# Optimization experiments

Measured on AMD Instinct MI355X. Metric: run time of the kernel, lower is better.

## Reference

```python
import jax, jax.numpy as jnp
import numpy as np

N = 4096          # batch size
D = 1024          # embedding dim
NUM_INSTANCES = 8 # samples per class (balanced batch, required by the original resize logic)
ALPHA = 20.0
MARGIN = 0.5


def setup_inputs() -> dict:
    key = jax.random.key(0)
    inputs = jax.random.normal(key, (N, D), dtype=jnp.float32)
    # balanced targets: each class appears exactly NUM_INSTANCES times
    targets = (jnp.arange(N, dtype=jnp.int32) // NUM_INSTANCES).astype(jnp.int32)
    return {"inputs": inputs, "targets": targets}


def reference(inputs, targets):
    n = inputs.shape[0]
    k_pos = NUM_INSTANCES - 1          # positives per row (excl. self)
    k_neg = n - NUM_INSTANCES          # negatives per row

    # L2 normalize rows, cosine similarity matrix [n, n]
    x = inputs / jnp.linalg.norm(inputs, axis=1, keepdims=True)
    sim = x @ x.T

    same = targets[:, None] == targets[None, :]
    eye = jnp.eye(n, dtype=bool)
    pos_mask = same & ~eye             # positives, diag removed
    neg_mask = ~same                   # negatives

    INF = jnp.float32(1e9)
    # per-row sorted positive / negative sims (ascending); fixed-size slices
    pos_sorted = jnp.sort(jnp.where(pos_mask, sim, INF), axis=1)[:, :k_pos]   # [n, k_pos]
    neg_sorted = jnp.sort(jnp.where(neg_mask, sim, INF), axis=1)[:, :k_neg]   # [n, k_neg]

    # base = max(max(sim) - 0.1, margin + 0.2)
    base = jnp.maximum(jnp.max(sim) - 0.1, MARGIN + 0.2)

    # dynamic selection expressed as masks over fixed-size sorted arrays
    neg_keep = neg_sorted > (pos_sorted[:, :1] - 0.05)   # negatives above min positive - 0.05
    pos_keep = pos_sorted < base                          # positives below base

    pos_elem = jnp.log1p(jnp.exp(-2.0 * (pos_sorted - MARGIN)))   # [n, k_pos]
    neg_elem = jnp.log1p(jnp.exp(ALPHA * (neg_sorted - MARGIN)))  # [n, k_neg]

    pos_cnt = pos_keep.sum(axis=1)
    neg_cnt = neg_keep.sum(axis=1)

    pos_mean = (pos_elem * pos_keep).sum(axis=1) / jnp.maximum(pos_cnt, 1).astype(sim.dtype)
    neg_mean = (neg_elem * neg_keep).sum(axis=1) / jnp.maximum(neg_cnt, 1).astype(sim.dtype)

    # fallbacks: empty pos set -> smallest positive; empty neg set -> largest negative
    pos_loss = jnp.where(pos_cnt > 0, pos_mean, pos_elem[:, 0])
    neg_loss = jnp.where(neg_cnt > 0, neg_mean, neg_elem[:, -1])

    return jnp.mean(pos_loss + neg_loss)   # sum over rows / n
```

## Files before the change

kernel.cpp:

```cpp
#include <hip/hip_runtime.h>
#include <hip/hip_bf16.h>
#include <hip/hip_fp8.h>
#include <math.h>

#define N 4096
#define D 1024
#define NINST 8
#define NGROUP (N / NINST)
#define ALPHA 20.0f
#define MARGIN 0.5f
#define NB 64
#define NTILE (NB * (NB + 1) / 2)

typedef __attribute__((ext_vector_type(4))) float f32x4;

__device__ __forceinline__ unsigned fkey(float f) {
    int b = __float_as_int(f);
    return (b >= 0) ? ((unsigned)b | 0x80000000u) : ~(unsigned)b;
}
__device__ __forceinline__ float fdec(unsigned u) {
    int b = (u & 0x80000000u) ? (int)(u ^ 0x80000000u) : ~(int)u;
    return __int_as_float(b);
}

__device__ __forceinline__ float softplus(float x) {
    float z = __expf(-fabsf(x));
    return fmaxf(x, 0.0f) + __logf(1.0f + z);
}

__device__ __forceinline__ void gld16(const void* g, void* l) {
    __builtin_amdgcn_global_load_lds(
        (const __attribute__((address_space(1))) void*)g,
        (__attribute__((address_space(3))) void*)l, 16, 0, 0);
}

__global__ __launch_bounds__(256) void k_normpos(const float* __restrict__ in,
                                                 unsigned long* __restrict__ xn8,
                                                 float* __restrict__ pos_sims,
                                                 float* __restrict__ min_pos,
                                                 unsigned* __restrict__ gmax,
                                                 float* __restrict__ accum,
                                                 unsigned* __restrict__ cnt) {
    __shared__ float4 srows4[8 * 257];
    __shared__ float spart[8][4];
    __shared__ float sinv[8];
    __shared__ float sg[8][8];

    int g = blockIdx.x;
    int t = threadIdx.x;
    int lane = t & 63, wid = t >> 6;

    if (g == 0) {
        if (t == 0) { *gmax = 0u; *cnt = 0u; }
        if (t < 32) accum[t] = 0.f;
    }

    const float4* in4 = (const float4*)in;
    #pragma unroll
    for (int i = 0; i < 8; ++i) {
        float4 v = in4[(size_t)g * 2048 + i * 256 + t];
        srows4[i * 257 + t] = v;
        float ss = v.x * v.x + v.y * v.y + v.z * v.z + v.w * v.w;
        #pragma unroll
        for (int off = 1; off < 64; off <<= 1) ss += __shfl_xor(ss, off);
        if (lane == 0) spart[i][wid] = ss;
    }
    __syncthreads();
    if (t < 8) sinv[t] = rsqrtf(spart[t][0] + spart[t][1] + spart[t][2] + spart[t][3]);
    __syncthreads();

    {
        int i_row = t & 7;
        int oct  = (t >> 3) & 3;
        int k0b  = t >> 5;
        size_t base = (size_t)(g >> 3) * 8192 + (size_t)((g >> 1) & 3) * 64
                    + (size_t)(oct * 16 + (g & 1) * 8 + i_row);
        float inv = sinv[i_row];
        #pragma unroll
        for (int j = 0; j < 4; ++j) {
            int k0 = k0b + j * 8;
            float4 v0 = srows4[i_row * 257 + k0 * 8 + oct * 2];
            float4 v1 = srows4[i_row * 257 + k0 * 8 + oct * 2 + 1];
            union { unsigned char c[8]; unsigned long u64; } o;
            o.c[0] = __hip_fp8_e4m3(v0.x * inv).__x;
            o.c[1] = __hip_fp8_e4m3(v0.y * inv).__x;
            o.c[2] = __hip_fp8_e4m3(v0.z * inv).__x;
            o.c[3] = __hip_fp8_e4m3(v0.w * inv).__x;
            o.c[4] = __hip_fp8_e4m3(v1.x * inv).__x;
            o.c[5] = __hip_fp8_e4m3(v1.y * inv).__x;
            o.c[6] = __hip_fp8_e4m3(v1.z * inv).__x;
            o.c[7] = __hip_fp8_e4m3(v1.w * inv).__x;
            xn8[base + (size_t)k0 * 256] = o.u64;
        }
    }

    int pair = t >> 2, a = pair >> 3, b = pair & 7, slice = t & 3;
    const float4* pa = srows4 + a * 257 + slice * 64;
    const float4* pb = srows4 + b * 257 + slice * 64;
    int j0 = (pair + slice * 2) & 63;
    float s = 0.f;
    #pragma unroll 8
    for (int i = 0; i < 64; ++i) {
        int j = (i + j0) & 63;
        float4 x = pa[j], y = pb[j];
        s += x.x * y.x + x.y * y.y + x.z * y.z + x.w * y.w;
    }
    s += __shfl_xor(s, 1);
    s += __shfl_xor(s, 2);
    if (slice == 0) sg[a][b] = s * sinv[a] * sinv[b];
    __syncthreads();
    if (t < 8) {
        float mn = 1e30f;
        int idx = 0;
        #pragma unroll
        for (int b2 = 0; b2 < 8; ++b2) {
            if (b2 == t) continue;
            float v = sg[t][b2];
            mn = fminf(mn, v);
            pos_sims[(size_t)(g * 8 + t) * 8 + idx] = v;
            ++idx;
        }
        min_pos[g * 8 + t] = mn;
    }
}

__global__ __launch_bounds__(256, 2) void k_neg(const unsigned long* __restrict__ xn8,
                                                const float* __restrict__ min_pos,
                                                float* __restrict__ sum_part,
                                                int* __restrict__ cnt_part,
                                                float* __restrict__ max_part,
                                                unsigned* __restrict__ gmax) {
    __shared__ char sbuf[4][3][4096];

    int t = threadIdx.x;
    int w = t >> 6;
    int l = t & 63;
    int u = blockIdx.x * 4 + w;

    int rt = 0, rem = u;
    while (rem >= NB - rt) { rem -= NB - rt; ++rt; }
    int ct = rt + rem;
    bool diag = (rt == ct);

    int R0 = rt * 64, C0 = ct * 64;
    int lrow = l & 15;
    int kgrp = l >> 4;

    float mA = min_pos[R0 + l];
    float mB = min_pos[C0 + l];
    asm volatile("s_waitcnt vmcnt(0)" ::: "memory");

    const char* xb = (const char*)xn8;
    const char* gA = xb + (size_t)rt * 65536 + (size_t)l * 16;
    const char* gB = xb + (size_t)ct * 65536 + (size_t)l * 16;
    char* ring = &sbuf[w][0][0];

    #define STAGE(s_)                                                   \
        do {                                                            \
            char* d_ = ring + ((s_) % 3) * 4096;                        \
            gld16(gA + (size_t)(s_) * 2048,        d_);                 \
            gld16(gA + (size_t)(s_) * 2048 + 1024, d_ + 1024);          \
            gld16(gB + (size_t)(s_) * 2048,        d_ + 2048);          \
            gld16(gB + (size_t)(s_) * 2048 + 1024, d_ + 3072);          \
        } while (0)

    STAGE(0); STAGE(1); STAGE(2);

    f32x4 zero = {0.f, 0.f, 0.f, 0.f};
    f32x4 acc[4][4];
    #pragma unroll
    for (int m = 0; m < 4; ++m)
        #pragma unroll
        for (int n = 0; n < 4; ++n) acc[m][n] = zero;

    for (int it = 0; it < 32; ++it) {
        if (it <= 29)      asm volatile("s_waitcnt vmcnt(8)" ::: "memory");
        else if (it == 30) asm volatile("s_waitcnt vmcnt(4)" ::: "memory");
        else               asm volatile("s_waitcnt vmcnt(0)" ::: "memory");

        const char* buf = ring + (it % 3) * 4096;
        long a[4], b[4];
        #pragma unroll
        for (int m = 0; m < 4; ++m) {
            a[m] = *(const long*)(buf + m * 512 + l * 8);
            b[m] = *(const long*)(buf + 2048 + m * 512 + l * 8);
        }

        #pragma unroll
        for (int m = 0; m < 4; ++m)
            #pragma unroll
            for (int n = 0; n < 4; ++n)
                acc[m][n] = __builtin_amdgcn_mfma_f32_16x16x32_fp8_fp8(
                    a[m], b[n], acc[m][n], 0, 0, 0);

        asm volatile("s_waitcnt lgkmcnt(0)" ::: "memory");
        if (it <= 28) STAGE(it + 3);
    }
    #undef STAGE

    float allmax = -1e30f;

    float thB[4];
    #pragma unroll
    for (int n = 0; n < 4; ++n) thB[n] = __shfl(mB, n * 16 + lrow) - 0.05f;

    float colS[4] = {0.f, 0.f, 0.f, 0.f};
    float colM[4] = {-1e30f, -1e30f, -1e30f, -1e30f};
    int   colC[4] = {0, 0, 0, 0};

    #pragma unroll
    for (int m = 0; m < 4; ++m) {
        #pragma unroll
        for (int reg = 0; reg < 4; ++reg) {
            int lr = m * 16 + kgrp * 4 + reg;
            int grow = R0 + lr;
            float th = __shfl(mA, lr) - 0.05f;
            int gi = grow >> 3;
            float rs = 0.f, rm = -1e30f;
            int rc = 0;
            #pragma unroll
            for (int n = 0; n < 4; ++n) {
                int gcol = C0 + n * 16 + lrow;
                float s = acc[m][n][reg];
                allmax = fmaxf(allmax, s);
                if ((gcol >> 3) != gi) {
                    float e = softplus(ALPHA * (s - MARGIN));
                    rm = fmaxf(rm, s);
                    if (s > th) { rs += e; rc += 1; }
                    if (!diag) {
                        colM[n] = fmaxf(colM[n], s);
                        if (s > thB[n]) { colS[n] += e; colC[n] += 1; }
                    }
                }
            }
            #pragma unroll
            for (int off = 1; off < 16; off <<= 1) {
                rs += __shfl_xor(rs, off);
                rc += __shfl_xor(rc, off);
                rm = fmaxf(rm, __shfl_xor(rm, off));
            }
            if (lrow == 0) {
                sum_part[(size_t)grow * 64 + ct] = rs;
                cnt_part[(size_t)grow * 64 + ct] = rc;
                max_part[(size_t)grow * 64 + ct] = rm;
            }
        }
    }

    if (!diag) {
        #pragma unroll
        for (int n = 0; n < 4; ++n) {
            float cs = colS[n], cm = colM[n];
            int cc = colC[n];
            cs += __shfl_xor(cs, 16); cs += __shfl_xor(cs, 32);
            cc += __shfl_xor(cc, 16); cc += __shfl_xor(cc, 32);
            cm = fmaxf(cm, __shfl_xor(cm, 16));
            cm = fmaxf(cm, __shfl_xor(cm, 32));
            if (kgrp == 0) {
                int gcol = C0 + n * 16 + lrow;
                sum_part[(size_t)gcol * 64 + rt] = cs;
                cnt_part[(size_t)gcol * 64 + rt] = cc;
                max_part[(size_t)gcol * 64 + rt] = cm;
            }
        }
    }

    #pragma unroll
    for (int off = 1; off < 64; off <<= 1) allmax = fmaxf(allmax, __shfl_xor(allmax, off));
    if (l == 0) atomicMax(gmax, fkey(allmax));
}

__global__ __launch_bounds__(256) void k_rowfinal(const float* __restrict__ sum_part,
                                                  const int* __restrict__ cnt_part,
                                                  const float* __restrict__ max_part,
                                                  const float* __restrict__ pos_sims,
                                                  const float* __restrict__ min_pos,
                                                  const unsigned* __restrict__ gmax,
                                                  float* __restrict__ accum,
                                                  unsigned* __restrict__ cnt,
                                                  float* __restrict__ out) {
    __shared__ float sloss[4];
    int row = blockIdx.x * 4 + (threadIdx.x >> 6);
    int lane = threadIdx.x & 63;
    float ns = sum_part[(size_t)row * 64 + lane];
    int nc = cnt_part[(size_t)row * 64 + lane];
    float nm = max_part[(size_t)row * 64 + lane];
    #pragma unroll
    for (int off = 1; off < 64; off <<= 1) {
        ns += __shfl_xor(ns, off);
        nc += __shfl_xor(nc, off);
        nm = fmaxf(nm, __shfl_xor(nm, off));
    }
    if (lane == 0) {
        float base = fmaxf(fdec(*gmax) - 0.1f, MARGIN + 0.2f);
        float neg_loss = (nc > 0) ? ns / (float)nc : softplus(ALPHA * (nm - MARGIN));
        float ps = 0.f;
        int pcnt = 0;
        float mn = min_pos[row];
        #pragma unroll
        for (int i = 0; i < NINST - 1; ++i) {
            float s = pos_sims[(size_t)row * 8 + i];
            if (s < base) { ps += softplus(-2.0f * (s - MARGIN)); pcnt++; }
        }
        float pos_loss = (pcnt > 0) ? ps / (float)pcnt : softplus(-2.0f * (mn - MARGIN));
        sloss[threadIdx.x >> 6] = pos_loss + neg_loss;
    }
    __syncthreads();
    if (threadIdx.x == 0) {
        float bs = sloss[0] + sloss[1] + sloss[2] + sloss[3];
        atomicAdd(&accum[blockIdx.x & 31], bs);
        __threadfence();
        unsigned old = atomicAdd(cnt, 1u);
        if (old == gridDim.x - 1) {
            __threadfence();
            float tot = 0.f;
            for (int j = 0; j < 32; ++j) tot += atomicAdd(&accum[j], 0.0f);
            out[0] = tot / (float)N;
        }
    }
}

extern "C" void kernel_launch(void* const* d_in, const int* in_sizes, int n_in,
                              void* d_out, int out_size, void* d_ws, size_t ws_size,
                              hipStream_t stream) {
    const float* in = (const float*)d_in[0];
    float* out = (float*)d_out;

    char* ws = (char*)d_ws;
    unsigned long* xn8 = (unsigned long*)(ws);
    float*   min_pos  = (float*)(ws + 8388608 + 16384);
    float*   pos_sims = (float*)(ws + 8388608 + 32768);
    float*   sum_part = (float*)(ws + 8388608 + 32768 + 131072);
    float*   max_part = (float*)(ws + 8388608 + 32768 + 131072 + 1048576);
    int*     cnt_part = (int*)  (ws + 8388608 + 32768 + 131072 + 2097152);
    unsigned* gmax    = (unsigned*)(ws + 8388608 + 32768 + 131072 + 3145728);
    float*   accum    = (float*)(ws + 8388608 + 32768 + 131072 + 3145728 + 128);
    unsigned* cnt     = (unsigned*)(ws + 8388608 + 32768 + 131072 + 3145728 + 256);

    k_normpos<<<NGROUP, 256, 0, stream>>>(in, xn8, pos_sims, min_pos, gmax, accum, cnt);
    k_neg<<<NTILE / 4, 256, 0, stream>>>(xn8, min_pos, sum_part, cnt_part, max_part, gmax);
    k_rowfinal<<<N / 4, 256, 0, stream>>>(sum_part, cnt_part, max_part, pos_sims, min_pos,
                                          gmax, accum, cnt, out);
}
```

Measured before the change: 100.1 us.

## Fuse three kernels into one persistent kernel with band counters and grid barrier

Merges normalization, the negative-tile MFMA pass and the row finalization into one persistent kernel of 512 blocks. Per-band atomic counters let tile work start as soon as its two row bands are normalized, and a software grid barrier separates tile work from the final reduction. This removes two kernel launch gaps and the tail idle time between stages. It adds a memset launch and spin-waiting, and it relies on all 512 blocks being co-resident at 2 blocks per CU to avoid deadlock.

After: 316.0 us. 3.16x slower.

```diff
diff --git a/kernel.cpp b/kernel.cpp
--- a/kernel.cpp
+++ b/kernel.cpp
@@ -11,6 +11,7 @@
 #define MARGIN 0.5f
 #define NB 64
 #define NTILE (NB * (NB + 1) / 2)
+#define NBLK 512
 
 typedef __attribute__((ext_vector_type(4))) float f32x4;
 
@@ -34,288 +35,309 @@
         (__attribute__((address_space(3))) void*)l, 16, 0, 0);
 }
 
-__global__ __launch_bounds__(256) void k_normpos(const float* __restrict__ in,
-                                                 unsigned long* __restrict__ xn8,
-                                                 float* __restrict__ pos_sims,
-                                                 float* __restrict__ min_pos,
-                                                 unsigned* __restrict__ gmax,
-                                                 float* __restrict__ accum,
-                                                 unsigned* __restrict__ cnt) {
-    __shared__ float4 srows4[8 * 257];
+__global__ __launch_bounds__(256, 2) void k_all(const float* __restrict__ in,
+                                                unsigned long* __restrict__ xn8,
+                                                float* __restrict__ pos_sims,
+                                                float* __restrict__ min_pos,
+                                                float* __restrict__ sum_part,
+                                                int* __restrict__ cnt_part,
+                                                float* __restrict__ max_part,
+                                                unsigned* __restrict__ ctrl,
+                                                float* __restrict__ accum,
+                                                float* __restrict__ out) {
+    __shared__ __align__(16) char smem[49152];
     __shared__ float spart[8][4];
     __shared__ float sinv[8];
     __shared__ float sg[8][8];
-
-    int g = blockIdx.x;
-    int t = threadIdx.x;
-    int lane = t & 63, wid = t >> 6;
-
-    if (g == 0) {
-        if (t == 0) { *gmax = 0u; *cnt = 0u; }
-        if (t < 32) accum[t] = 0.f;
-    }
-
-    const float4* in4 = (const float4*)in;
-    #pragma unroll
-    for (int i = 0; i < 8; ++i) {
-        float4 v = in4[(size_t)g * 2048 + i * 256 + t];
-        srows4[i * 257 + t] = v;
-        float ss = v.x * v.x + v.y * v.y + v.z * v.z + v.w * v.w;
-        #pragma unroll
-        for (int off = 1; off < 64; off <<= 1) ss += __shfl_xor(ss, off);
-        if (lane == 0) spart[i][wid] = ss;
-    }
-    __syncthreads();
-    if (t < 8) sinv[t] = rsqrtf(spart[t][0] + spart[t][1] + spart[t][2] + spart[t][3]);
-    __syncthreads();
-
-    {
-        int i_row = t & 7;
-        int oct  = (t >> 3) & 3;
-        int k0b  = t >> 5;
-        size_t base = (size_t)(g >> 3) * 8192 + (size_t)((g >> 1) & 3) * 64
-                    + (size_t)(oct * 16 + (g & 1) * 8 + i_row);
-        float inv = sinv[i_row];
-        #pragma unroll
-        for (int j = 0; j < 4; ++j) {
-            int k0 = k0b + j * 8;
-            float4 v0 = srows4[i_row * 257 + k0 * 8 + oct * 2];
-            float4 v1 = srows4[i_row * 257 + k0 * 8 + oct * 2 + 1];
-            union { unsigned char c[8]; unsigned long u64; } o;
-            o.c[0] = __hip_fp8_e4m3(v0.x * inv).__x;
-            o.c[1] = __hip_fp8_e4m3(v0.y * inv).__x;
-            o.c[2] = __hip_fp8_e4m3(v0.z * inv).__x;
-            o.c[3] = __hip_fp8_e4m3(v0.w * inv).__x;
-            o.c[4] = __hip_fp8_e4m3(v1.x * inv).__x;
-            o.c[5] = __hip_fp8_e4m3(v1.y * inv).__x;
-            o.c[6] = __hip_fp8_e4m3(v1.z * inv).__x;
-            o.c[7] = __hip_fp8_e4m3(v1.w * inv).__x;
-            xn8[base + (size_t)k0 * 256] = o.u64;
-        }
-    }
-
-    int pair = t >> 2, a = pair >> 3, b = pair & 7, slice = t & 3;
-    const float4* pa = srows4 + a * 257 + slice * 64;
-    const float4* pb = srows4 + b * 257 + slice * 64;
-    int j0 = (pair + slice * 2) & 63;
-    float s = 0.f;
-    #pragma unroll 8
-    for (int i = 0; i < 64; ++i) {
-        int j = (i + j0) & 63;
-        float4 x = pa[j], y = pb[j];
-        s += x.x * y.x + x.y * y.y + x.z * y.z + x.w * y.w;
-    }
-    s += __shfl_xor(s, 1);
-    s += __shfl_xor(s, 2);
-    if (slice == 0) sg[a][b] = s * sinv[a] * sinv[b];
-    __syncthreads();
-    if (t < 8) {
-        float mn = 1e30f;
-        int idx = 0;
-        #pragma unroll
-        for (int b2 = 0; b2 < 8; ++b2) {
-            if (b2 == t) continue;
-            float v = sg[t][b2];
-            mn = fminf(mn, v);
-            pos_sims[(size_t)(g * 8 + t) * 8 + idx] = v;
-            ++idx;
-        }
-        min_pos[g * 8 + t] = mn;
-    }
-}
-
-__global__ __launch_bounds__(256, 2) void k_neg(const unsigned long* __restrict__ xn8,
-                                                const float* __restrict__ min_pos,
-                                                float* __restrict__ sum_part,
-                                                int* __restrict__ cnt_part,
-                                                float* __restrict__ max_part,
-                                                unsigned* __restrict__ gmax) {
-    __shared__ char sbuf[4][3][4096];
-
+    __shared__ float sloss[8];
+
+    unsigned* gmax     = ctrl + 0;
+    unsigned* sem2     = ctrl + 1;
+    unsigned* cnt3     = ctrl + 2;
+    unsigned* band_cnt = ctrl + 4;
+
+    int bid = blockIdx.x;
     int t = threadIdx.x;
     int w = t >> 6;
     int l = t & 63;
-    int u = blockIdx.x * 4 + w;
-
-    int rt = 0, rem = u;
-    while (rem >= NB - rt) { rem -= NB - rt; ++rt; }
-    int ct = rt + rem;
-    bool diag = (rt == ct);
-
-    int R0 = rt * 64, C0 = ct * 64;
-    int lrow = l & 15;
-    int kgrp = l >> 4;
-
-    float mA = min_pos[R0 + l];
-    float mB = min_pos[C0 + l];
-    asm volatile("s_waitcnt vmcnt(0)" ::: "memory");
-
-    const char* xb = (const char*)xn8;
-    const char* gA = xb + (size_t)rt * 65536 + (size_t)l * 16;
-    const char* gB = xb + (size_t)ct * 65536 + (size_t)l * 16;
-    char* ring = &sbuf[w][0][0];
-
-    #define STAGE(s_)                                                   \
-        do {                                                            \
-            char* d_ = ring + ((s_) % 3) * 4096;                        \
-            gld16(gA + (size_t)(s_) * 2048,        d_);                 \
-            gld16(gA + (size_t)(s_) * 2048 + 1024, d_ + 1024);          \
-            gld16(gB + (size_t)(s_) * 2048,        d_ + 2048);          \
-            gld16(gB + (size_t)(s_) * 2048 + 1024, d_ + 3072);          \
-        } while (0)
-
-    STAGE(0); STAGE(1); STAGE(2);
-
-    f32x4 zero = {0.f, 0.f, 0.f, 0.f};
-    f32x4 acc[4][4];
-    #pragma unroll
-    for (int m = 0; m < 4; ++m)
+
+    {
+        int g = bid;
+        int lane = l, wid = w;
+        float4* srows4 = (float4*)smem;
+
+        const float4* in4 = (const float4*)in;
         #pragma unroll
-        for (int n = 0; n < 4; ++n) acc[m][n] = zero;
-
-    for (int it = 0; it < 32; ++it) {
-        if (it <= 29)      asm volatile("s_waitcnt vmcnt(8)" ::: "memory");
-        else if (it == 30) asm volatile("s_waitcnt vmcnt(4)" ::: "memory");
-        else               asm volatile("s_waitcnt vmcnt(0)" ::: "memory");
-
-        const char* buf = ring + (it % 3) * 4096;
-        long a[4], b[4];
-        #pragma unroll
-        for (int m = 0; m < 4; ++m) {
-            a[m] = *(const long*)(buf + m * 512 + l * 8);
-            b[m] = *(const long*)(buf + 2048 + m * 512 + l * 8);
-        }
-
-        #pragma unroll
-        for (int m = 0; m < 4; ++m)
-            #pragma unroll
-            for (int n = 0; n < 4; ++n)
-                acc[m][n] = __builtin_amdgcn_mfma_f32_16x16x32_fp8_fp8(
-                    a[m], b[n], acc[m][n], 0, 0, 0);
-
-        asm volatile("s_waitcnt lgkmcnt(0)" ::: "memory");
-        if (it <= 28) STAGE(it + 3);
+        for (int i = 0; i < 8; ++i) {
+            float4 v = in4[(size_t)g * 2048 + i * 256 + t];
+            srows4[i * 257 + t] = v;
+            float ss = v.x * v.x + v.y * v.y + v.z * v.z + v.w * v.w;
+            #pragma unroll
+            for (int off = 1; off < 64; off <<= 1) ss += __shfl_xor(ss, off);
+            if (lane == 0) spart[i][wid] = ss;
+        }
+        __syncthreads();
+        if (t < 8) sinv[t] = rsqrtf(spart[t][0] + spart[t][1] + spart[t][2] + spart[t][3]);
+        __syncthreads();
+
+        {
+            int i_row = t & 7;
+            int oct  = (t >> 3) & 3;
+            int k0b  = t >> 5;
+            size_t base = (size_t)(g >> 3) * 8192 + (size_t)((g >> 1) & 3) * 64
+                        + (size_t)(oct * 16 + (g & 1) * 8 + i_row);
+            float inv = sinv[i_row];
+            #pragma unroll
+            for (int j = 0; j < 4; ++j) {
+                int k0 = k0b + j * 8;
+                float4 v0 = srows4[i_row * 257 + k0 * 8 + oct * 2];
+                float4 v1 = srows4[i_row * 257 + k0 * 8 + oct * 2 + 1];
+                union { unsigned char c[8]; unsigned long u64; } o;
+                o.c[0] = __hip_fp8_e4m3(v0.x * inv).__x;
+                o.c[1] = __hip_fp8_e4m3(v0.y * inv).__x;
+                o.c[2] = __hip_fp8_e4m3(v0.z * inv).__x;
+                o.c[3] = __hip_fp8_e4m3(v0.w * inv).__x;
+                o.c[4] = __hip_fp8_e4m3(v1.x * inv).__x;
+                o.c[5] = __hip_fp8_e4m3(v1.y * inv).__x;
+                o.c[6] = __hip_fp8_e4m3(v1.z * inv).__x;
+                o.c[7] = __hip_fp8_e4m3(v1.w * inv).__x;
+                xn8[base + (size_t)k0 * 256] = o.u64;
+            }
+        }
+
+        int pair = t >> 2, a = pair >> 3, b = pair & 7, slice = t & 3;
+        const float4* pa = srows4 + a * 257 + slice * 64;
+        const float4* pb = srows4 + b * 257 + slice * 64;
+        int j0 = (pair + slice * 2) & 63;
+        float s = 0.f;
+        #pragma unroll 8
+        for (int i = 0; i < 64; ++i) {
+            int j = (i + j0) & 63;
+            float4 x = pa[j], y = pb[j];
+            s += x.x * y.x + x.y * y.y + x.z * y.z + x.w * y.w;
+        }
+        s += __shfl_xor(s, 1);
+        s += __shfl_xor(s, 2);
+        if (slice == 0) sg[a][b] = s * sinv[a] * sinv[b];
+        __syncthreads();
+        if (t < 8) {
+            float mn = 1e30f;
+            int idx = 0;
+            #pragma unroll
+            for (int b2 = 0; b2 < 8; ++b2) {
+                if (b2 == t) continue;
+                float v = sg[t][b2];
+                mn = fminf(mn, v);
+                pos_sims[(size_t)(g * 8 + t) * 8 + idx] = v;
+                ++idx;
+            }
+            min_pos[g * 8 + t] = mn;
+        }
+        __syncthreads();
+        __threadfence();
+        if (t == 0)
+            __hip_atomic_fetch_add(&band_cnt[bid >> 3], 1u,
+                                   __ATOMIC_RELAXED, __HIP_MEMORY_SCOPE_AGENT);
     }
-    #undef STAGE
-
-    float allmax = -1e30f;
-
-    float thB[4];
-    #pragma unroll
-    for (int n = 0; n < 4; ++n) thB[n] = __shfl(mB, n * 16 + lrow) - 0.05f;
-
-    float colS[4] = {0.f, 0.f, 0.f, 0.f};
-    float colM[4] = {-1e30f, -1e30f, -1e30f, -1e30f};
-    int   colC[4] = {0, 0, 0, 0};
-
-    #pragma unroll
-    for (int m = 0; m < 4; ++m) {
-        #pragma unroll
-        for (int reg = 0; reg < 4; ++reg) {
-            int lr = m * 16 + kgrp * 4 + reg;
-            int grow = R0 + lr;
-            float th = __shfl(mA, lr) - 0.05f;
-            int gi = grow >> 3;
-            float rs = 0.f, rm = -1e30f;
-            int rc = 0;
-            #pragma unroll
-            for (int n = 0; n < 4; ++n) {
-                int gcol = C0 + n * 16 + lrow;
-                float s = acc[m][n][reg];
-                allmax = fmaxf(allmax, s);
-                if ((gcol >> 3) != gi) {
-                    float e = softplus(ALPHA * (s - MARGIN));
-                    rm = fmaxf(rm, s);
-                    if (s > th) { rs += e; rc += 1; }
-                    if (!diag) {
-                        colM[n] = fmaxf(colM[n], s);
-                        if (s > thB[n]) { colS[n] += e; colC[n] += 1; }
+    __syncthreads();
+
+    {
+        int lrow = l & 15;
+        int kgrp = l >> 4;
+        char* ring = smem + w * 12288;
+
+        for (int u = bid * 4 + w; u < NTILE; u += 4 * NBLK) {
+            int rt = 0, rem = u;
+            while (rem >= NB - rt) { rem -= NB - rt; ++rt; }
+            int ct = rt + rem;
+            bool diag = (rt == ct);
+            int R0 = rt * 64, C0 = ct * 64;
+
+            if (l == 0) {
+                while (__hip_atomic_load(&band_cnt[rt], __ATOMIC_RELAXED,
+                                         __HIP_MEMORY_SCOPE_AGENT) < 8u ||
+                       __hip_atomic_load(&band_cnt[ct], __ATOMIC_RELAXED,
+                                         __HIP_MEMORY_SCOPE_AGENT) < 8u)
+                    __builtin_amdgcn_s_sleep(8);
+            }
+            __threadfence();
+
+            float mA = min_pos[R0 + l];
+            float mB = min_pos[C0 + l];
+            asm volatile("s_waitcnt vmcnt(0)" ::: "memory");
+
+            const char* xb = (const char*)xn8;
+            const char* gA = xb + (size_t)rt * 65536 + (size_t)l * 16;
+            const char* gB = xb + (size_t)ct * 65536 + (size_t)l * 16;
+
+            #define STAGE(s_)                                                   \
+                do {                                                            \
+                    char* d_ = ring + ((s_) % 3) * 4096;                        \
+                    gld16(gA + (size_t)(s_) * 2048,        d_);                 \
+                    gld16(gA + (size_t)(s_) * 2048 + 1024, d_ + 1024);          \
+                    gld16(gB + (size_t)(s_) * 2048,        d_ + 2048);          \
+                    gld16(gB + (size_t)(s_) * 2048 + 1024, d_ + 3072);          \
+                } while (0)
+
+            STAGE(0); STAGE(1); STAGE(2);
+
+            f32x4 zero = {0.f, 0.f, 0.f, 0.f};
+            f32x4 acc[4][4];
+            #pragma unroll
+            for (int m = 0; m < 4; ++m)
+                #pragma unroll
+                for (int n = 0; n < 4; ++n) acc[m][n] = zero;
+
+            for (int it = 0; it < 32; ++it) {
+                if (it <= 29)      asm volatile("s_waitcnt vmcnt(8)" ::: "memory");
+                else if (it == 30) asm volatile("s_waitcnt vmcnt(4)" ::: "memory");
+                else               asm volatile("s_waitcnt vmcnt(0)" ::: "memory");
+
+                const char* buf = ring + (it % 3) * 4096;
+                long a[4], b[4];
+                #pragma unroll
+                for (int m = 0; m < 4; ++m) {
+                    a[m] = *(const long*)(buf + m * 512 + l * 8);
+                    b[m] = *(const long*)(buf + 2048 + m * 512 + l * 8);
+                }
+
+                #pragma unroll
+                for (int m = 0; m < 4; ++m)
+                    #pragma unroll
+                    for (int n = 0; n < 4; ++n)
+                        acc[m][n] = __builtin_amdgcn_mfma_f32_16x16x32_fp8_fp8(
+                            a[m], b[n], acc[m][n], 0, 0, 0);
+
+                asm volatile("s_waitcnt lgkmcnt(0)" ::: "memory");
+                if (it <= 28) STAGE(it + 3);
+            }
+            #undef STAGE
+
+            float allmax = -1e30f;
+            float thB[4];
+            #pragma unroll
+            for (int n = 0; n < 4; ++n) thB[n] = __shfl(mB, n * 16 + lrow) - 0.05f;
+
+            float colS[4] = {0.f, 0.f, 0.f, 0.f};
+            float colM[4] = {-1e30f, -1e30f, -1e30f, -1e30f};
+            int   colC[4] = {0, 0, 0, 0};
+
+            #pragma unroll
+            for (int m = 0; m < 4; ++m) {
+                #pragma unroll
+                for (int reg = 0; reg < 4; ++reg) {
+                    int lr = m * 16 + kgrp * 4 + reg;
+                    int grow = R0 + lr;
+                    float th = __shfl(mA, lr) - 0.05f;
+                    int gi = grow >> 3;
+                    float rs = 0.f, rm = -1e30f;
+                    int rc = 0;
+                    #pragma unroll
+                    for (int n = 0; n < 4; ++n) {
+                        int gcol = C0 + n * 16 + lrow;
+                        float s = acc[m][n][reg];
+                        allmax = fmaxf(allmax, s);
+                        if ((gcol >> 3) != gi) {
+                            float e = softplus(ALPHA * (s - MARGIN));
+                            rm = fmaxf(rm, s);
+                            if (s > th) { rs += e; rc += 1; }
+                            if (!diag) {
+                                colM[n] = fmaxf(colM[n], s);
+                                if (s > thB[n]) { colS[n] += e; colC[n] += 1; }
+                            }
+                        }
+                    }
+                    #pragma unroll
+                    for (int off = 1; off < 16; off <<= 1) {
+                        rs += __shfl_xor(rs, off);
+                        rc += __shfl_xor(rc, off);
+                        rm = fmaxf(rm, __shfl_xor(rm, off));
+                    }
+                    if (lrow == 0) {
+                        sum_part[(size_t)grow * 64 + ct] = rs;
+                        cnt_part[(size_t)grow * 64 + ct] = rc;
+                        max_part[(size_t)grow * 64 + ct] = rm;
                     }
                 }
             }
-            #pragma unroll
-            for (int off = 1; off < 16; off <<= 1) {
-                rs += __shfl_xor(rs, off);
-                rc += __shfl_xor(rc, off);
-                rm = fmaxf(rm, __shfl_xor(rm, off));
-            }
-            if (lrow == 0) {
-                sum_part[(size_t)grow * 64 + ct] = rs;
-                cnt_part[(size_t)grow * 64 + ct] = rc;
-                max_part[(size_t)grow * 64 + ct] = rm;
-            }
+
+            if (!diag) {
+                #pragma unroll
+                for (int n = 0; n < 4; ++n) {
+                    float cs = colS[n], cm = colM[n];
+                    int cc = colC[n];
+                    cs += __shfl_xor(cs, 16); cs += __shfl_xor(cs, 32);
+                    cc += __shfl_xor(cc, 16); cc += __shfl_xor(cc, 32);
+                    cm = fmaxf(cm, __shfl_xor(cm, 16));
+                    cm = fmaxf(cm, __shfl_xor(cm, 32));
+                    if (kgrp == 0) {
+                        int gcol = C0 + n * 16 + lrow;
+                        sum_part[(size_t)gcol * 64 + rt] = cs;
+                        cnt_part[(size_t)gcol * 64 + rt] = cc;
+                        max_part[(size_t)gcol * 64 + rt] = cm;
+                    }
+                }
+            }
+
+            #pragma unroll
+            for (int off = 1; off < 64; off <<= 1) allmax = fmaxf(allmax, __shfl_xor(allmax, off));
+            if (l == 0) atomicMax(gmax, fkey(allmax));
         }
     }
 
-    if (!diag) {
-        #pragma unroll
-        for (int n = 0; n < 4; ++n) {
-            float cs = colS[n], cm = colM[n];
-            int cc = colC[n];
-            cs += __shfl_xor(cs, 16); cs += __shfl_xor(cs, 32);
-            cc += __shfl_xor(cc, 16); cc += __shfl_xor(cc, 32);
-            cm = fmaxf(cm, __shfl_xor(cm, 16));
-            cm = fmaxf(cm, __shfl_xor(cm, 32));
-            if (kgrp == 0) {
-                int gcol = C0 + n * 16 + lrow;
-                sum_part[(size_t)gcol * 64 + rt] = cs;
-                cnt_part[(size_t)gcol * 64 + rt] = cc;
-                max_part[(size_t)gcol * 64 + rt] = cm;
-            }
-        }
-    }
-
-    #pragma unroll
-    for (int off = 1; off < 64; off <<= 1) allmax = fmaxf(allmax, __shfl_xor(allmax, off));
-    if (l == 0) atomicMax(gmax, fkey(allmax));
-}
-
-__global__ __launch_bounds__(256) void k_rowfinal(const float* __restrict__ sum_part,
-                                                  const int* __restrict__ cnt_part,
-                                                  const float* __restrict__ max_part,
-                                                  const float* __restrict__ pos_sims,
-                                                  const float* __restrict__ min_pos,
-                                                  const unsigned* __restrict__ gmax,
-                                                  float* __restrict__ accum,
-                                                  unsigned* __restrict__ cnt,
-                                                  float* __restrict__ out) {
-    __shared__ float sloss[4];
-    int row = blockIdx.x * 4 + (threadIdx.x >> 6);
-    int lane = threadIdx.x & 63;
-    float ns = sum_part[(size_t)row * 64 + lane];
-    int nc = cnt_part[(size_t)row * 64 + lane];
-    float nm = max_part[(size_t)row * 64 + lane];
-    #pragma unroll
-    for (int off = 1; off < 64; off <<= 1) {
-        ns += __shfl_xor(ns, off);
-        nc += __shfl_xor(nc, off);
-        nm = fmaxf(nm, __shfl_xor(nm, off));
-    }
-    if (lane == 0) {
-        float base = fmaxf(fdec(*gmax) - 0.1f, MARGIN + 0.2f);
-        float neg_loss = (nc > 0) ? ns / (float)nc : softplus(ALPHA * (nm - MARGIN));
-        float ps = 0.f;
-        int pcnt = 0;
-        float mn = min_pos[row];
-        #pragma unroll
-        for (int i = 0; i < NINST - 1; ++i) {
-            float s = pos_sims[(size_t)row * 8 + i];
-            if (s < base) { ps += softplus(-2.0f * (s - MARGIN)); pcnt++; }
-        }
-        float pos_loss = (pcnt > 0) ? ps / (float)pcnt : softplus(-2.0f * (mn - MARGIN));
-        sloss[threadIdx.x >> 6] = pos_loss + neg_loss;
+    __syncthreads();
+    __threadfence();
+    if (t == 0)
+        __hip_atomic_fetch_add(sem2, 1u, __ATOMIC_RELAXED, __HIP_MEMORY_SCOPE_AGENT);
+    if (t == 0) {
+        while (__hip_atomic_load(sem2, __ATOMIC_RELAXED, __HIP_MEMORY_SCOPE_AGENT) < (unsigned)NBLK)
+            __builtin_amdgcn_s_sleep(8);
     }
     __syncthreads();
-    if (threadIdx.x == 0) {
-        float bs = sloss[0] + sloss[1] + sloss[2] + sloss[3];
-        atomicAdd(&accum[blockIdx.x & 31], bs);
-        __threadfence();
-        unsigned old = atomicAdd(cnt, 1u);
-        if (old == gridDim.x - 1) {
+    __threadfence();
+
+    {
+        float base = fmaxf(fdec(*gmax) - 0.1f, MARGIN + 0.2f);
+        #pragma unroll
+        for (int rr = 0; rr < 2; ++rr) {
+            int row = bid * 8 + w * 2 + rr;
+            float ns = sum_part[(size_t)row * 64 + l];
+            int nc = cnt_part[(size_t)row * 64 + l];
+            float nm = max_part[(size_t)row * 64 + l];
+            #pragma unroll
+            for (int off = 1; off < 64; off <<= 1) {
+                ns += __shfl_xor(ns, off);
+                nc += __shfl_xor(nc, off);
+                nm = fmaxf(nm, __shfl_xor(nm, off));
+            }
+            if (l == 0) {
+                float neg_loss = (nc > 0) ? ns / (float)nc : softplus(ALPHA * (nm - MARGIN));
+                float ps = 0.f;
+                int pcnt = 0;
+                float mn = min_pos[row];
+                #pragma unroll
+                for (int i = 0; i < NINST - 1; ++i) {
+                    float s = pos_sims[(size_t)row * 8 + i];
+                    if (s < base) { ps += softplus(-2.0f * (s - MARGIN)); pcnt++; }
+                }
+                float pos_loss = (pcnt > 0) ? ps / (float)pcnt : softplus(-2.0f * (mn - MARGIN));
+                sloss[w * 2 + rr] = pos_loss + neg_loss;
+            }
+        }
+        __syncthreads();
+        if (t == 0) {
+            float bs = 0.f;
+            #pragma unroll
+            for (int i = 0; i < 8; ++i) bs += sloss[i];
+            atomicAdd(&accum[bid & 31], bs);
             __threadfence();
-            float tot = 0.f;
-            for (int j = 0; j < 32; ++j) tot += atomicAdd(&accum[j], 0.0f);
-            out[0] = tot / (float)N;
+            unsigned old = atomicAdd(cnt3, 1u);
+            if (old == (unsigned)(NBLK - 1)) {
+                __threadfence();
+                float tot = 0.f;
+                for (int j = 0; j < 32; ++j) tot += atomicAdd(&accum[j], 0.0f);
+                out[0] = tot / (float)N;
+            }
         }
     }
 }
@@ -333,12 +355,12 @@
     float*   sum_part = (float*)(ws + 8388608 + 32768 + 131072);
     float*   max_part = (float*)(ws + 8388608 + 32768 + 131072 + 1048576);
     int*     cnt_part = (int*)  (ws + 8388608 + 32768 + 131072 + 2097152);
-    unsigned* gmax    = (unsigned*)(ws + 8388608 + 32768 + 131072 + 3145728);
-    float*   accum    = (float*)(ws + 8388608 + 32768 + 131072 + 3145728 + 128);
-    unsigned* cnt     = (unsigned*)(ws + 8388608 + 32768 + 131072 + 3145728 + 256);
-
-    k_normpos<<<NGROUP, 256, 0, stream>>>(in, xn8, pos_sims, min_pos, gmax, accum, cnt);
-    k_neg<<<NTILE / 4, 256, 0, stream>>>(xn8, min_pos, sum_part, cnt_part, max_part, gmax);
-    k_rowfinal<<<N / 4, 256, 0, stream>>>(sum_part, cnt_part, max_part, pos_sims, min_pos,
-                                          gmax, accum, cnt, out);
-}
+    unsigned* ctrl    = (unsigned*)(ws + 8388608 + 32768 + 131072 + 3145728);
+    float*   accum    = (float*)(ws + 8388608 + 32768 + 131072 + 3145728 + 384);
+
+    hipMemsetAsync(ctrl, 0, 512, stream);
+
+    k_all<<<NBLK, 256, 0, stream>>>(in, xn8, pos_sims, min_pos,
+                                    sum_part, cnt_part, max_part,
+                                    ctrl, accum, out);
+}
```
